# Kernel optimization log

Measured on AMD Instinct MI355X. Metric: run time of the kernel, lower is better.

The kernel has to match this reference:

```python
import jax, jax.numpy as jnp
import numpy as np

NUM_EXPERT = 16
IN_FEAT = 1024
OUT_FEAT = 4096
N_TOKENS = 2048


def setup_inputs() -> dict:
    key = jax.random.key(0)
    k1, k2, k3 = jax.random.split(key, 3)
    inp = jax.random.normal(k1, (N_TOKENS, IN_FEAT), dtype=jnp.float32)
    gate = jax.random.randint(k2, (N_TOKENS,), 0, NUM_EXPERT, dtype=jnp.int32)
    # reset_parameters() fills each expert with nn.Linear weights:
    # kaiming-uniform, effectively U(-1/sqrt(in_feat), 1/sqrt(in_feat))
    bound = 1.0 / np.sqrt(IN_FEAT)
    weight = jax.random.uniform(
        k3, (NUM_EXPERT, OUT_FEAT, IN_FEAT), dtype=jnp.float32,
        minval=-bound, maxval=bound)
    return {"inp": inp, "gate": gate, "weight": weight}


def reference(inp, gate, weight):
    # Grouped GEMM: out[n] = weight[gate[n]] @ inp[n]
    # Expressed as dense one-hot dispatch -> per-expert GEMM -> combine,
    # which computes the identical math without materializing a per-token
    # [N, out, in] gathered weight tensor.
    onehot = jax.nn.one_hot(gate, NUM_EXPERT, dtype=inp.dtype)       # [N, E]
    dispatched = jnp.einsum('ne,nd->end', onehot, inp)               # [E, N, in]
    expert_out = jnp.einsum('end,eod->eno', dispatched, weight)      # [E, N, out]
    out = jnp.einsum('ne,eno->no', onehot, expert_out)               # [N, out]
    return out
```

## Files before the change

### kernel.cpp

```cpp
#include <hip/hip_runtime.h>
#include <hip/hip_bf16.h>

#define NEXP 16
#define KDIM 1024
#define ODIM 4096
#define NTOK 2048

#define BM   256
#define BN   256
#define KC   32
#define NPH  (KDIM / KC)
#define NBLK (NEXP * (ODIM / BN))

#define WS(s) ((s) * 32768)
#define AS(s) (98304 + (s) * 16384)
#define LDS_BYTES (3 * 32768 + 3 * 16384)

typedef __attribute__((ext_vector_type(8))) short short8;
typedef __attribute__((ext_vector_type(4))) float f32x4;

typedef __attribute__((address_space(3))) unsigned lds_uint;
typedef const __attribute__((address_space(1))) unsigned glob_uint;

__device__ __forceinline__ void gload16(const void* g, void* l) {
    __builtin_amdgcn_global_load_lds((glob_uint*)g, (lds_uint*)l, 16, 0, 0);
}

__device__ __forceinline__ unsigned short f2bf(float f) {
    __hip_bfloat16 h = __float2bfloat16(f);
    return __builtin_bit_cast(unsigned short, h);
}

__device__ __forceinline__ short8 pack8(float4 a, float4 b) {
    short8 r;
    r[0] = (short)f2bf(a.x); r[1] = (short)f2bf(a.y);
    r[2] = (short)f2bf(a.z); r[3] = (short)f2bf(a.w);
    r[4] = (short)f2bf(b.x); r[5] = (short)f2bf(b.y);
    r[6] = (short)f2bf(b.z); r[7] = (short)f2bf(b.w);
    return r;
}

__device__ __forceinline__ short8 pack8v(f32x4 a, f32x4 b) {
    short8 r;
    r[0] = (short)f2bf(a[0]); r[1] = (short)f2bf(a[1]);
    r[2] = (short)f2bf(a[2]); r[3] = (short)f2bf(a[3]);
    r[4] = (short)f2bf(b[0]); r[5] = (short)f2bf(b[1]);
    r[6] = (short)f2bf(b[2]); r[7] = (short)f2bf(b[3]);
    return r;
}

#define SFENCE() __builtin_amdgcn_sched_barrier(0)
#define WAITVM(N) do { SFENCE(); \
        asm volatile("s_waitcnt vmcnt(" #N ")" ::: "memory"); SFENCE(); } while (0)
#define BAR() do { SFENCE(); __builtin_amdgcn_s_barrier(); SFENCE(); } while (0)

__global__ __launch_bounds__(256) void moe_sort(const int* __restrict__ gate,
                                                int* __restrict__ perm,
                                                int* __restrict__ offs) {
    __shared__ int lgate[NTOK];
    __shared__ int hist[256][NEXP + 1];
    __shared__ int base[NEXP];
    const int t = threadIdx.x;
    for (int i = t; i < NTOK; i += 256) lgate[i] = gate[i];
    #pragma unroll
    for (int e = 0; e < NEXP; ++e) hist[t][e] = 0;
    __syncthreads();
    const int TPT = NTOK / 256;
    for (int j = 0; j < TPT; ++j) hist[t][lgate[t * TPT + j]]++;
    __syncthreads();
    if (t < NEXP) {
        int s = 0;
        for (int i = 0; i < 256; ++i) { int v = hist[i][t]; hist[i][t] = s; s += v; }
        base[t] = s;
    }
    __syncthreads();
    if (t == 0) {
        int s = 0;
        for (int e = 0; e < NEXP; ++e) { int v = base[e]; base[e] = s; offs[e] = s; s += v; }
        offs[NEXP] = s;
    }
    __syncthreads();
    #pragma unroll
    for (int e = 0; e < NEXP; ++e) hist[t][e] += base[e];
    for (int j = 0; j < TPT; ++j) {
        int tok = t * TPT + j;
        int e = lgate[tok];
        int pos = hist[t][e]++;
        perm[pos] = tok;
    }
}

__global__ __launch_bounds__(256) void moe_cvt(const float* __restrict__ inp,
                                               const int* __restrict__ perm,
                                               unsigned short* __restrict__ A2T2) {
    const int o   = blockIdx.x;
    const int pos = blockIdx.y * 256 + threadIdx.x;
    const int tok = perm[pos];
    const float4* s = (const float4*)(inp + (size_t)tok * KDIM + o * 8);
    float4 v0 = s[0], v1 = s[1];
    *(short8*)(A2T2 + ((size_t)o * NTOK + pos) * 8) = pack8(v0, v1);
}

template <bool PRE>
__global__ __launch_bounds__(1024, 4) void moe_gemm(
    const float* __restrict__ inp,
    const unsigned short* __restrict__ A2T2,
    const float* __restrict__ weight,
    const int* __restrict__ perm,
    const int* __restrict__ offs,
    float* __restrict__ out)
{
    const int bid = blockIdx.x;
    const int v   = (bid & 7) * (NBLK / 8) + (bid >> 3);
    const int e   = v >> 4;
    const int oc  = (v & 15) * BN;

    const int beg = offs[e], end = offs[e + 1];
    const int nall = end - beg;
    if (nall <= 0) return;

    __shared__ char lds[LDS_BYTES];

    const int t    = threadIdx.x;
    const int lane = t & 63;
    const int w    = t >> 6;
    const int wm   = w >> 3;
    const int wn   = w & 7;
    const int frow = lane & 15;
    const int fks  = lane >> 4;

    const int wrow = t >> 3;
    const int hs   = (t & 7) ^ ((t >> 3) & 7);
    const float* bsrc0 = weight + ((size_t)e * ODIM + oc + wrow) * KDIM + hs * 4;
    const float* bsrc1 = bsrc0 + (size_t)128 * KDIM;

#define ISSUE_W(s, p) {                                                       \
        gload16(bsrc0 + (p) * KC, lds + WS(s) + t * 16);                      \
        gload16(bsrc1 + (p) * KC, lds + WS(s) + 16384 + t * 16);              \
    }
#define ISSUE_A(s, p) {                                                       \
        gload16(asrcB + (size_t)(p) * (4 * NTOK * 8), lds + AS(s) + t * 16);  \
    }
#define STEP(s) {                                                             \
        const char* Wb = lds + WS(s);                                         \
        const char* Ab = lds + AS(s);                                         \
        int rB = wn * 32 + frow;                                              \
        const int x = frow & 7;                                               \
        f32x4 lo = *(const f32x4*)(Wb + (rB * 8 + ((2 * fks)     ^ x)) * 16); \
        f32x4 hi = *(const f32x4*)(Wb + (rB * 8 + ((2 * fks + 1) ^ x)) * 16); \
        short8 bf0 = pack8v(lo, hi);                                          \
        rB += 16;                                                             \
        lo = *(const f32x4*)(Wb + (rB * 8 + ((2 * fks)     ^ x)) * 16);       \
        hi = *(const f32x4*)(Wb + (rB * 8 + ((2 * fks + 1) ^ x)) * 16);       \
        short8 bf1 = pack8v(lo, hi);                                          \
        _Pragma("unroll")                                                     \
        for (int m = 0; m < 8; ++m) {                                         \
            if (m * 16 < mmax) {                                              \
                short8 af = *(const short8*)(Ab +                             \
                    (fks * 256 + wm * 128 + m * 16 + frow) * 16);             \
                acc[m][0] = __builtin_amdgcn_mfma_f32_16x16x32_bf16(af, bf0, acc[m][0], 0, 0, 0); \
                acc[m][1] = __builtin_amdgcn_mfma_f32_16x16x32_bf16(af, bf1, acc[m][1], 0, 0, 0); \
            }                                                                 \
        }                                                                     \
    }

    for (int base = 0; base < nall; base += BM) {
        const int rows = (nall - base < BM) ? (nall - base) : BM;
        const int c0   = beg + base;
        const int mmax = rows - wm * 128;

        int rcl = t & 255; if (rcl > rows - 1) rcl = rows - 1;
        const unsigned short* asrcB =
            A2T2 + ((size_t)(t >> 8) * NTOK + (c0 + rcl)) * 8;
        const float* afsrc = PRE ? 0
            : inp + (size_t)perm[c0 + rcl] * KDIM + (t >> 8) * 8;

        f32x4 acc[8][2];
        #pragma unroll
        for (int m = 0; m < 8; ++m) {
            acc[m][0] = (f32x4){0.f, 0.f, 0.f, 0.f};
            acc[m][1] = (f32x4){0.f, 0.f, 0.f, 0.f};
        }

        __syncthreads();

        if (PRE) {
            ISSUE_W(0, 0); ISSUE_A(0, 0);
            ISSUE_W(1, 1); ISSUE_A(1, 1);
            WAITVM(3);
            BAR();
            int s0 = 0, s1 = 1, s2 = 2;
            for (int p = 0; p < NPH; ++p) {
                if (p + 2 < NPH) { ISSUE_W(s2, p + 2); ISSUE_A(s2, p + 2); SFENCE(); }
                STEP(s0);
                if (p + 2 < NPH)      { WAITVM(3); }
                else if (p + 1 < NPH) { WAITVM(0); }
                if (p + 1 < NPH) BAR();
                int tmp = s0; s0 = s1; s1 = s2; s2 = tmp;
            }
        } else {
            for (int p = 0; p < NPH; ++p) {
                float4 a0 = *(const float4*)(afsrc + p * KC);
                float4 a1 = *(const float4*)(afsrc + p * KC + 4);
                ISSUE_W(0, p);
                __syncthreads();
                *(short8*)(lds + AS(0) + t * 16) = pack8(a0, a1);
                WAITVM(0);
                __syncthreads();
                STEP(0);
            }
        }

        const int col0 = oc + wn * 32 + frow;
        #pragma unroll
        for (int m = 0; m < 8; ++m) {
            #pragma unroll
            for (int reg = 0; reg < 4; ++reg) {
                int r = wm * 128 + m * 16 + fks * 4 + reg;
                if (r < rows) {
                    int tok = perm[c0 + r];
                    float* orow = out + (size_t)tok * ODIM + col0;
                    orow[0]  = acc[m][0][reg];
                    orow[16] = acc[m][1][reg];
                }
            }
        }
    }
#undef ISSUE_W
#undef ISSUE_A
#undef STEP
}

extern "C" void kernel_launch(void* const* d_in, const int* in_sizes, int n_in,
                              void* d_out, int out_size, void* d_ws, size_t ws_size,
                              hipStream_t stream) {
    const float* inp    = (const float*)d_in[0];
    const int*   gate   = (const int*)d_in[1];
    const float* weight = (const float*)d_in[2];
    float*       out    = (float*)d_out;

    int* perm = (int*)d_ws;
    int* offs = perm + NTOK;
    unsigned short* A2T2 = (unsigned short*)((char*)d_ws + 16384);
    const size_t need = 16384 + (size_t)NTOK * KDIM * 2 + 65536;
    const bool pre = (ws_size >= need);

    moe_sort<<<1, 256, 0, stream>>>(gate, perm, offs);
    if (pre) {
        dim3 cg(KDIM / 8, NTOK / 256);
        moe_cvt<<<cg, 256, 0, stream>>>(inp, perm, A2T2);
        moe_gemm<true><<<NBLK, 1024, 0, stream>>>(inp, A2T2, weight, perm, offs, out);
    } else {
        moe_gemm<false><<<NBLK, 1024, 0, stream>>>(inp, A2T2, weight, perm, offs, out);
    }
}
```

Measured before the change: 95.71 us.

## Shrink token tile to 160 and double-buffer 64-wide weight chunks

Reduces the M tile from 256 to 160 rows, so the typical ~128-token expert group wastes fewer MFMA slots and accumulator registers. Weight tiles are now staged in 64-wide K chunks with two buffers, and activations keep a three-stage ring of 32-wide chunks. This halves the number of weight-load issue and wait points and reworks the swizzle and wait counts. In exchange the kernel uses more LDS (about 158 KB) and more complex vmcnt accounting, and 384 of the 1024 threads now sit idle during activation staging.

```diff
diff --git a/kernel.cpp b/kernel.cpp
--- a/kernel.cpp
+++ b/kernel.cpp
@@ -6,15 +6,16 @@
 #define ODIM 4096
 #define NTOK 2048
 
-#define BM   256
+#define BM   160
 #define BN   256
 #define KC   32
+#define KC2  64
 #define NPH  (KDIM / KC)
 #define NBLK (NEXP * (ODIM / BN))
 
-#define WS(s) ((s) * 32768)
-#define AS(s) (98304 + (s) * 16384)
-#define LDS_BYTES (3 * 32768 + 3 * 16384)
+#define WS(s) ((s) * 65536)
+#define AS(s) (131072 + (s) * 10240)
+#define LDS_BYTES 161792
 
 typedef __attribute__((ext_vector_type(8))) short short8;
 typedef __attribute__((ext_vector_type(4))) float f32x4;
@@ -129,35 +130,45 @@
     const int frow = lane & 15;
     const int fks  = lane >> 4;
 
-    const int wrow = t >> 3;
-    const int hs   = (t & 7) ^ ((t >> 3) & 7);
-    const float* bsrc0 = weight + ((size_t)e * ODIM + oc + wrow) * KDIM + hs * 4;
-    const float* bsrc1 = bsrc0 + (size_t)128 * KDIM;
-
-#define ISSUE_W(s, p) {                                                       \
-        gload16(bsrc0 + (p) * KC, lds + WS(s) + t * 16);                      \
-        gload16(bsrc1 + (p) * KC, lds + WS(s) + 16384 + t * 16);              \
+    const float* bsrc[4];
+    #pragma unroll
+    for (int q = 0; q < 4; ++q) {
+        int g = t + q * 1024;
+        int row = g >> 4, slot = g & 15;
+        bsrc[q] = weight + ((size_t)e * ODIM + oc + row) * KDIM
+                  + (slot ^ (row & 15)) * 4;
+    }
+    const bool astage = (t < 640);
+    const int aoct = t / 160;
+    const int apos = t - aoct * 160;
+
+#define ISSUE_W(s, ks2) {                                                     \
+        _Pragma("unroll")                                                     \
+        for (int q = 0; q < 4; ++q)                                           \
+            gload16(bsrc[q] + (ks2) * KC2, lds + WS(s) + (t + q * 1024) * 16);\
     }
 #define ISSUE_A(s, p) {                                                       \
-        gload16(asrcB + (size_t)(p) * (4 * NTOK * 8), lds + AS(s) + t * 16);  \
-    }
-#define STEP(s) {                                                             \
-        const char* Wb = lds + WS(s);                                         \
-        const char* Ab = lds + AS(s);                                         \
+        if (astage)                                                           \
+            gload16(asrcB + (size_t)(p) * (4 * NTOK * 8),                     \
+                    lds + AS(s) + t * 16);                                    \
+    }
+#define STEP(sw, q, sa) {                                                     \
+        const char* Wb = lds + WS(sw);                                        \
+        const char* Ab = lds + AS(sa);                                        \
         int rB = wn * 32 + frow;                                              \
-        const int x = frow & 7;                                               \
-        f32x4 lo = *(const f32x4*)(Wb + (rB * 8 + ((2 * fks)     ^ x)) * 16); \
-        f32x4 hi = *(const f32x4*)(Wb + (rB * 8 + ((2 * fks + 1) ^ x)) * 16); \
+        const int x = rB & 15;                                                \
+        f32x4 lo = *(const f32x4*)(Wb + (rB * 16 + (((q)*8 + 2*fks)     ^ x)) * 16); \
+        f32x4 hi = *(const f32x4*)(Wb + (rB * 16 + (((q)*8 + 2*fks + 1) ^ x)) * 16); \
         short8 bf0 = pack8v(lo, hi);                                          \
         rB += 16;                                                             \
-        lo = *(const f32x4*)(Wb + (rB * 8 + ((2 * fks)     ^ x)) * 16);       \
-        hi = *(const f32x4*)(Wb + (rB * 8 + ((2 * fks + 1) ^ x)) * 16);       \
+        lo = *(const f32x4*)(Wb + (rB * 16 + (((q)*8 + 2*fks)     ^ x)) * 16);\
+        hi = *(const f32x4*)(Wb + (rB * 16 + (((q)*8 + 2*fks + 1) ^ x)) * 16);\
         short8 bf1 = pack8v(lo, hi);                                          \
         _Pragma("unroll")                                                     \
-        for (int m = 0; m < 8; ++m) {                                         \
+        for (int m = 0; m < 5; ++m) {                                         \
             if (m * 16 < mmax) {                                              \
                 short8 af = *(const short8*)(Ab +                             \
-                    (fks * 256 + wm * 128 + m * 16 + frow) * 16);             \
+                    (fks * BM + wm * 80 + m * 16 + frow) * 16);               \
                 acc[m][0] = __builtin_amdgcn_mfma_f32_16x16x32_bf16(af, bf0, acc[m][0], 0, 0, 0); \
                 acc[m][1] = __builtin_amdgcn_mfma_f32_16x16x32_bf16(af, bf1, acc[m][1], 0, 0, 0); \
             }                                                                 \
@@ -167,17 +178,15 @@
     for (int base = 0; base < nall; base += BM) {
         const int rows = (nall - base < BM) ? (nall - base) : BM;
         const int c0   = beg + base;
-        const int mmax = rows - wm * 128;
-
-        int rcl = t & 255; if (rcl > rows - 1) rcl = rows - 1;
+        const int mmax = rows - wm * 80;
+
+        int rcl = apos; if (rcl > rows - 1) rcl = rows - 1;
         const unsigned short* asrcB =
-            A2T2 + ((size_t)(t >> 8) * NTOK + (c0 + rcl)) * 8;
-        const float* afsrc = PRE ? 0
-            : inp + (size_t)perm[c0 + rcl] * KDIM + (t >> 8) * 8;
-
-        f32x4 acc[8][2];
+            A2T2 + ((size_t)aoct * NTOK + (c0 + rcl)) * 8;
+
+        f32x4 acc[5][2];
         #pragma unroll
-        for (int m = 0; m < 8; ++m) {
+        for (int m = 0; m < 5; ++m) {
             acc[m][0] = (f32x4){0.f, 0.f, 0.f, 0.f};
             acc[m][1] = (f32x4){0.f, 0.f, 0.f, 0.f};
         }
@@ -185,38 +194,56 @@
         __syncthreads();
 
         if (PRE) {
-            ISSUE_W(0, 0); ISSUE_A(0, 0);
-            ISSUE_W(1, 1); ISSUE_A(1, 1);
-            WAITVM(3);
+            ISSUE_A(0, 0);
+            ISSUE_A(1, 1);
+            ISSUE_W(0, 0);
+            WAITVM(0);
             BAR();
-            int s0 = 0, s1 = 1, s2 = 2;
+            int sa0 = 0, sa1 = 1, sa2 = 2;
+            for (int j = 0; j < 15; ++j) {
+                const int sw = j & 1;
+                ISSUE_A(sa2, 2 * j + 2);
+                ISSUE_W(sw ^ 1, j + 1);
+                SFENCE();
+                STEP(sw, 0, sa0);
+                if (astage) { WAITVM(5); }
+                BAR();
+                { int tmp = sa0; sa0 = sa1; sa1 = sa2; sa2 = tmp; }
+                ISSUE_A(sa2, 2 * j + 3);
+                SFENCE();
+                STEP(sw, 1, sa0);
+                if (astage) { WAITVM(1); }
+                else        { WAITVM(0); }
+                BAR();
+                { int tmp = sa0; sa0 = sa1; sa1 = sa2; sa2 = tmp; }
+            }
+            STEP(1, 0, sa0);
+            WAITVM(0);
+            BAR();
+            { int tmp = sa0; sa0 = sa1; sa1 = sa2; sa2 = tmp; }
+            STEP(1, 1, sa0);
+        } else {
+            const float* afsrc = inp + (size_t)perm[c0 + rcl] * KDIM + aoct * 8;
             for (int p = 0; p < NPH; ++p) {
-                if (p + 2 < NPH) { ISSUE_W(s2, p + 2); ISSUE_A(s2, p + 2); SFENCE(); }
-                STEP(s0);
-                if (p + 2 < NPH)      { WAITVM(3); }
-                else if (p + 1 < NPH) { WAITVM(0); }
-                if (p + 1 < NPH) BAR();
-                int tmp = s0; s0 = s1; s1 = s2; s2 = tmp;
-            }
-        } else {
-            for (int p = 0; p < NPH; ++p) {
-                float4 a0 = *(const float4*)(afsrc + p * KC);
-                float4 a1 = *(const float4*)(afsrc + p * KC + 4);
-                ISSUE_W(0, p);
                 __syncthreads();
-                *(short8*)(lds + AS(0) + t * 16) = pack8(a0, a1);
+                if ((p & 1) == 0) ISSUE_W(0, p >> 1);
+                if (astage) {
+                    float4 a0 = *(const float4*)(afsrc + p * KC);
+                    float4 a1 = *(const float4*)(afsrc + p * KC + 4);
+                    *(short8*)(lds + AS(0) + t * 16) = pack8(a0, a1);
+                }
                 WAITVM(0);
                 __syncthreads();
-                STEP(0);
+                STEP(0, p & 1, 0);
             }
         }
 
         const int col0 = oc + wn * 32 + frow;
         #pragma unroll
-        for (int m = 0; m < 8; ++m) {
+        for (int m = 0; m < 5; ++m) {
             #pragma unroll
             for (int reg = 0; reg < 4; ++reg) {
-                int r = wm * 128 + m * 16 + fks * 4 + reg;
+                int r = wm * 80 + m * 16 + fks * 4 + reg;
                 if (r < rows) {
                     int tok = perm[c0 + r];
                     float* orow = out + (size_t)tok * ODIM + col0;
```

After: 87.78 us. -8.3%, faster.
